# Kernel optimization log

Hardware: AMD Instinct MI355X
Metric: run time of the kernel (lower is better)

## Reference

```python
import jax, jax.numpy as jnp
import numpy as np

N_NODES = 50000
N_EDGES = 800000
N_FEAT = 128
N_HID = 256
N_PAIRS = 100000


def _gcn_norm(edge_index, n_nodes):
    # add self loops, compute D^-1/2 (A+I) D^-1/2 edge weights (PyG gcn_norm)
    loops = jnp.arange(n_nodes, dtype=edge_index.dtype)
    row = jnp.concatenate([edge_index[0], loops])
    col = jnp.concatenate([edge_index[1], loops])
    deg = jax.ops.segment_sum(jnp.ones_like(col, dtype=jnp.float32), col,
                              num_segments=n_nodes)
    dinv = jnp.where(deg > 0, jax.lax.rsqrt(deg), 0.0)
    norm = dinv[row] * dinv[col]  # [E + N]
    return row, col, norm


def _gcn_conv(x, W, b, row, col, norm, n_nodes):
    h = x @ W                       # [N, out]
    msg = h[row] * norm[:, None]    # gather + scale  [E+N, out]
    agg = jax.ops.segment_sum(msg, col, num_segments=n_nodes)  # scatter-add
    return agg + b


def setup_inputs() -> dict:
    key = jax.random.key(0)
    ks = jax.random.split(key, 9)
    edge_index = jax.random.randint(ks[0], (2, N_EDGES), 0, N_NODES, dtype=jnp.int64)
    features = jax.random.normal(ks[1], (N_NODES, N_FEAT), dtype=jnp.float32)
    mask = jax.random.randint(ks[2], (N_PAIRS, 2), 0, N_NODES, dtype=jnp.int64)
    s1 = 1.0 / np.sqrt(N_FEAT)
    s2 = 1.0 / np.sqrt(N_HID)
    W1 = jax.random.uniform(ks[3], (N_FEAT, N_HID), jnp.float32, -s1, s1)
    b1 = jnp.zeros((N_HID,), jnp.float32)
    W2 = jax.random.uniform(ks[4], (N_HID, N_FEAT), jnp.float32, -s2, s2)
    b2 = jnp.zeros((N_FEAT,), jnp.float32)
    Wl = jax.random.uniform(ks[5], (N_HID, 1), jnp.float32, -s2, s2)
    bl = jax.random.uniform(ks[6], (1,), jnp.float32, -s2, s2)
    return {"edge_index": edge_index, "features": features, "mask": mask,
            "W1": W1, "b1": b1, "W2": W2, "b2": b2, "Wl": Wl, "bl": bl}


def reference(edge_index, features, mask, W1, b1, W2, b2, Wl, bl):
    n = features.shape[0]
    row, col, norm = _gcn_norm(edge_index, n)
    h = _gcn_conv(features, W1, b1, row, col, norm, n)   # GCNConv a
    h = jax.nn.relu(h)                                   # dropout p=0 -> identity
    h = _gcn_conv(h, W2, b2, row, col, norm, n)          # GCNConv b
    mt = mask.T
    p1 = jax.lax.stop_gradient(h[mt[0]])                 # .detach()
    p2 = jax.lax.stop_gradient(h[mt[1]])
    hp = jnp.concatenate([p1, p2], axis=1)               # [n_pairs, 2*n_feat]
    return jax.nn.sigmoid(hp @ Wl + bl)
```

## Files before the change

### kernel.cpp

```cpp
#include <hip/hip_runtime.h>
#include <math.h>

#define NFEAT 128
#define NHID 256
#define NBLK 256

typedef __attribute__((ext_vector_type(8))) short short8;
typedef __attribute__((ext_vector_type(4))) float f32x4;
typedef __attribute__((ext_vector_type(2))) float f32x2;

__device__ inline unsigned short f2bf(float f) {
  unsigned u = __float_as_uint(f);
  u += 0x7fffu + ((u >> 16) & 1u);
  return (unsigned short)(u >> 16);
}
__device__ inline float bflo(unsigned u) { return __uint_as_float(u << 16); }
__device__ inline float bfhi(unsigned u) { return __uint_as_float(u & 0xffff0000u); }


__device__ inline void packOne(const float* __restrict__ W,
                               unsigned short* __restrict__ Wp, int idx, int KS,
                               int OUT) {
  int lane = idx & 63;
  int t = idx >> 6;
  int ks = t % KS;
  int nt = t / KS;
  int n = nt * 16 + (lane & 15);
  int k0 = ks * 32 + (lane >> 4) * 8;
  unsigned short v[8];
#pragma unroll
  for (int j = 0; j < 8; j++) v[j] = f2bf(W[(size_t)(k0 + j) * OUT + n]);
  *reinterpret_cast<short8*>(Wp + (size_t)idx * 8) =
      *reinterpret_cast<short8*>(v);
}

__global__ __launch_bounds__(1024) void k_hist_pack(
    const int* __restrict__ col, int* __restrict__ hist2d, int nE, int nb,
    const float* __restrict__ W1, const float* __restrict__ W2,
    unsigned short* __restrict__ W1p, unsigned short* __restrict__ W2p) {
  if (blockIdx.x >= NBLK) {
    int idx = (blockIdx.x - NBLK) * 1024 + threadIdx.x;
    if (idx < 4096) packOne(W1, W1p, idx, 4, 256);
    else packOne(W2, W2p, idx - 4096, 8, 128);
    return;
  }
  __shared__ int h[1024];
  for (int i = threadIdx.x; i < nb; i += 1024) h[i] = 0;
  __syncthreads();
  int chunk = (nE + NBLK - 1) / NBLK;
  int beg = blockIdx.x * chunk, end = min(beg + chunk, nE);
  for (int e = beg + threadIdx.x; e < end; e += 1024)
    atomicAdd(&h[col[e] >> 6], 1);
  __syncthreads();
  for (int i = threadIdx.x; i < nb; i += 1024)
    hist2d[i * NBLK + blockIdx.x] = h[i];
}

__global__ __launch_bounds__(256) void k_bsum(const int* __restrict__ a,
                                              int* __restrict__ psum, int S,
                                              const float* __restrict__ b2,
                                              const float* __restrict__ Wl,
                                              const float* __restrict__ bl,
                                              float* __restrict__ Cbuf) {
  int t = threadIdx.x;
  if (blockIdx.x == gridDim.x - 1) {
    float v = (t < 128) ? b2[t] * (Wl[t] + Wl[128 + t]) : 0.f;
#pragma unroll
    for (int o = 32; o; o >>= 1) v += __shfl_down(v, o);
    __shared__ float fw[4];
    if ((t & 63) == 0) fw[t >> 6] = v;
    __syncthreads();
    if (t == 0) Cbuf[0] = fw[0] + fw[1] + fw[2] + fw[3] + bl[0];
    return;
  }
  int i = blockIdx.x * 256 + t;
  int v = (i < S) ? a[i] : 0;
#pragma unroll
  for (int o = 32; o; o >>= 1) v += __shfl_down(v, o);
  __shared__ int ws[4];
  if ((t & 63) == 0) ws[t >> 6] = v;
  __syncthreads();
  if (t == 0) psum[blockIdx.x] = ws[0] + ws[1] + ws[2] + ws[3];
}

__global__ __launch_bounds__(256) void k_s3m(const int* __restrict__ a,
                                             const int* __restrict__ psum,
                                             int* __restrict__ out, int S) {
  __shared__ int sh[256];
  __shared__ int ws[4];
  int t = threadIdx.x;
  int b = blockIdx.x;
  int partial = 0;
  for (int i = t; i < b; i += 256) partial += psum[i];
#pragma unroll
  for (int o = 32; o; o >>= 1) partial += __shfl_down(partial, o);
  if ((t & 63) == 0) ws[t >> 6] = partial;
  int i = b * 256 + t;
  int d = (i < S) ? a[i] : 0;
  sh[t] = d;
  __syncthreads();
  int base = ws[0] + ws[1] + ws[2] + ws[3];
  for (int o = 1; o < 256; o <<= 1) {
    int u = (t >= o) ? sh[t - o] : 0;
    __syncthreads();
    sh[t] += u;
    __syncthreads();
  }
  if (i < S) out[i] = base + sh[t] - d;
}

__global__ __launch_bounds__(1024) void k_part2(const int* __restrict__ row,
                                                const int* __restrict__ col,
                                                const int* __restrict__ sbase,
                                                unsigned* __restrict__ tmp,
                                                int nE, int nb) {
  __shared__ int cur[1024];
  for (int i = threadIdx.x; i < nb; i += 1024)
    cur[i] = sbase[i * NBLK + blockIdx.x];
  __syncthreads();
  int chunk = (nE + NBLK - 1) / NBLK;
  int beg = blockIdx.x * chunk, end = min(beg + chunk, nE);
  for (int e = beg + threadIdx.x; e < end; e += 1024) {
    int c = col[e];
    int pos = atomicAdd(&cur[c >> 6], 1);
    tmp[pos] = ((unsigned)(c & 63) << 16) | (unsigned)row[e];
  }
}

__global__ __launch_bounds__(256) void k_bsort_cvt(
    const unsigned* __restrict__ tmp, const int* __restrict__ sbase,
    int* __restrict__ ebuf, int* __restrict__ offs, float* __restrict__ dinv,
    const float* __restrict__ feat, unsigned short* __restrict__ xs, int n,
    int nE, int nb) {
  __shared__ int bins[4][64], cur4[4][64];
  __shared__ float sdinv[64];
  int b = blockIdx.x;
  int beg = sbase[b * NBLK];
  int end = (b == nb - 1) ? nE : sbase[(b + 1) * NBLK];
  int t = threadIdx.x;
  int w4 = t >> 6;
  if (t == 0 && b == nb - 1) offs[n] = nE;
  bins[w4][t & 63] = 0;
  __syncthreads();
  for (int i = beg + t; i < end; i += 256)
    atomicAdd(&bins[w4][tmp[i] >> 16], 1);
  __syncthreads();
  if (t < 64) {
    int b0 = bins[0][t], b1 = bins[1][t], b2 = bins[2][t], b3 = bins[3][t];
    int v = b0 + b1 + b2 + b3;
    int s = v;
#pragma unroll
    for (int o = 1; o < 64; o <<= 1) {
      int u = __shfl_up(s, o);
      if (t >= o) s += u;
    }
    int off = beg + s - v;
    cur4[0][t] = off;
    cur4[1][t] = off + b0;
    cur4[2][t] = off + b0 + b1;
    cur4[3][t] = off + b0 + b1 + b2;
    float dv = rsqrtf((float)(v + 1));
    sdinv[t] = dv;
    int node = b * 64 + t;
    if (node < n) {
      offs[node] = off;
      dinv[node] = dv;
    }
  }
  __syncthreads();
  for (int i = beg + t; i < end; i += 256) {
    unsigned p = tmp[i];
    int pos = atomicAdd(&cur4[w4][p >> 16], 1);
    ebuf[pos] = (int)(p & 0xffffu);
  }
  for (int i = t; i < 64 * 32; i += 256) {
    int r = i >> 5;
    int node = b * 64 + r;
    if (node >= n) break;
    float d = sdinv[r];
    float4 v = reinterpret_cast<const float4*>(feat)[(size_t)node * 32 + (i & 31)];
    unsigned short o[4] = {f2bf(v.x * d), f2bf(v.y * d), f2bf(v.z * d),
                           f2bf(v.w * d)};
    reinterpret_cast<ushort4*>(xs)[(size_t)node * 32 + (i & 31)] =
        *reinterpret_cast<ushort4*>(o);
  }
}

#define ACC2(A, V)                        \
  A[0] += (f32x2){bflo(V.x), bfhi(V.x)};  \
  A[1] += (f32x2){bflo(V.y), bfhi(V.y)};  \
  A[2] += (f32x2){bflo(V.z), bfhi(V.z)};  \
  A[3] += (f32x2){bflo(V.w), bfhi(V.w)};

__global__ __launch_bounds__(256) void k_fused(
    const char* __restrict__ Gb, const int* __restrict__ offs,
    const int* __restrict__ ebuf, const float* __restrict__ dinv,
    const unsigned short* __restrict__ B1p, const unsigned short* __restrict__ B2p,
    const float* __restrict__ b1, const float* __restrict__ Wl,
    float* __restrict__ P, int n) {
  __shared__ __align__(16) unsigned short sh[32 * 264];
  __shared__ float pacc[32][2];
  int rt0 = blockIdx.x * 2;
  int wave = threadIdx.x >> 6;
  int lane = threadIdx.x & 63;
  int quad = lane >> 4;
  if (threadIdx.x < 64) pacc[threadIdx.x >> 1][threadIdx.x & 1] = 0.f;

  {
    int g = lane >> 4;
    int cidx = lane & 15;
    unsigned cb = (unsigned)cidx << 4;
    int rbase = rt0 * 16;
    for (int it = 0; it < 8; ++it) {
      int rin = wave * 8 + it;
      int node = rbase + rin;
      f32x2 acc[4] = {};
      float d = 0.f;
      if (node < n) {
        d = dinv[node];
        int beg = offs[node], end = offs[node + 1];
        int deg = end - beg;
        if (g == 0) {
          uint4 s = *reinterpret_cast<const uint4*>(
              Gb + (((unsigned)node << 8) | cb));
          ACC2(acc, s);
        }
        int kb = 0;
        while (kb < deg) {
          int m = min(deg - kb, 64);
          int myi = beg + kb + lane;
          int idx = (myi < end) ? ebuf[myi] : 0;
          int j = 0;
          for (; j + 16 <= m; j += 16) {
            int s0 = __shfl(idx, j + g);
            int s1 = __shfl(idx, j + 4 + g);
            int s2 = __shfl(idx, j + 8 + g);
            int s3 = __shfl(idx, j + 12 + g);
            uint4 v0 = *reinterpret_cast<const uint4*>(Gb + (((unsigned)s0 << 8) | cb));
            uint4 v1 = *reinterpret_cast<const uint4*>(Gb + (((unsigned)s1 << 8) | cb));
            uint4 v2 = *reinterpret_cast<const uint4*>(Gb + (((unsigned)s2 << 8) | cb));
            uint4 v3 = *reinterpret_cast<const uint4*>(Gb + (((unsigned)s3 << 8) | cb));
            ACC2(acc, v0);
            ACC2(acc, v1);
            ACC2(acc, v2);
            ACC2(acc, v3);
          }
          for (; j + 4 <= m; j += 4) {
            int s0 = __shfl(idx, j + g);
            uint4 v0 = *reinterpret_cast<const uint4*>(Gb + (((unsigned)s0 << 8) | cb));
            ACC2(acc, v0);
          }
          int r = m - j;
          if (r > 0) {
            int s0 = __shfl(idx, j + ((g < r) ? g : 0));
            if (g < r) {
              uint4 v0 = *reinterpret_cast<const uint4*>(Gb + (((unsigned)s0 << 8) | cb));
              ACC2(acc, v0);
            }
          }
          kb += 64;
        }
      }
#pragma unroll
      for (int j = 0; j < 4; j++) {
        acc[j].x += __shfl_down(acc[j].x, 32);
        acc[j].y += __shfl_down(acc[j].y, 32);
        acc[j].x += __shfl_down(acc[j].x, 16);
        acc[j].y += __shfl_down(acc[j].y, 16);
      }
      if (g == 0) {
        unsigned o[4];
#pragma unroll
        for (int k = 0; k < 4; k++)
          o[k] = (unsigned)f2bf(acc[k].x * d) |
                 ((unsigned)f2bf(acc[k].y * d) << 16);
        *reinterpret_cast<uint4*>(sh + rin * 128 + (cidx ^ (rin & 7)) * 8) =
            *reinterpret_cast<uint4*>(o);
      }
    }
  }
  __syncthreads();

  int r0a = lane & 15;
  int xsw = lane & 7;
  short8 fa0[4], fa1[4];
#pragma unroll
  for (int ks = 0; ks < 4; ks++) {
    int cS = ((quad + ks * 4) ^ xsw) * 8;
    fa0[ks] = *reinterpret_cast<const short8*>(sh + r0a * 128 + cS);
    fa1[ks] = *reinterpret_cast<const short8*>(sh + (16 + r0a) * 128 + cS);
  }
  __syncthreads();

  f32x4 acc[2][4] = {};
#pragma unroll
  for (int ks = 0; ks < 4; ks++) {
#pragma unroll
    for (int ct = 0; ct < 4; ct++) {
      int nt = wave * 4 + ct;
      short8 b = *reinterpret_cast<const short8*>(
          B1p + ((size_t)(nt * 4 + ks) * 64 + lane) * 8);
      acc[0][ct] = __builtin_amdgcn_mfma_f32_16x16x32_bf16(fa0[ks], b, acc[0][ct], 0, 0, 0);
      acc[1][ct] = __builtin_amdgcn_mfma_f32_16x16x32_bf16(fa1[ks], b, acc[1][ct], 0, 0, 0);
    }
  }
#pragma unroll
  for (int ct = 0; ct < 4; ct++) {
    int c = (wave * 4 + ct) * 16 + (lane & 15);
    float bv = b1[c];
#pragma unroll
    for (int rg = 0; rg < 2; rg++)
#pragma unroll
      for (int i = 0; i < 4; i++) {
        float v = fmaxf(acc[rg][ct][i] + bv, 0.f);
        sh[(rg * 16 + quad * 4 + i) * 264 + c] = f2bf(v);
      }
  }
  __syncthreads();

  f32x4 acc2[2][2] = {};
  const unsigned short* a2_0 = sh + (size_t)(lane & 15) * 264 + quad * 8;
  const unsigned short* a2_1 = sh + (size_t)(16 + (lane & 15)) * 264 + quad * 8;
#pragma unroll
  for (int ks = 0; ks < 8; ks++) {
    short8 a0 = *reinterpret_cast<const short8*>(a2_0 + ks * 32);
    short8 a1 = *reinterpret_cast<const short8*>(a2_1 + ks * 32);
#pragma unroll
    for (int ct = 0; ct < 2; ct++) {
      int nt = wave * 2 + ct;
      short8 b = *reinterpret_cast<const short8*>(
          B2p + ((size_t)(nt * 8 + ks) * 64 + lane) * 8);
      acc2[0][ct] = __builtin_amdgcn_mfma_f32_16x16x32_bf16(a0, b, acc2[0][ct], 0, 0, 0);
      acc2[1][ct] = __builtin_amdgcn_mfma_f32_16x16x32_bf16(a1, b, acc2[1][ct], 0, 0, 0);
    }
  }
  float p1[2][4] = {}, p2[2][4] = {};
#pragma unroll
  for (int rg = 0; rg < 2; rg++) {
    int r0 = (rt0 + rg) * 16 + quad * 4;
    float dv[4];
#pragma unroll
    for (int i = 0; i < 4; i++) dv[i] = dinv[r0 + i];
#pragma unroll
    for (int ct = 0; ct < 2; ct++) {
      int c = (wave * 2 + ct) * 16 + (lane & 15);
      float wl1 = Wl[c], wl2 = Wl[128 + c];
#pragma unroll
      for (int i = 0; i < 4; i++) {
        float v = acc2[rg][ct][i] * dv[i];
        p1[rg][i] = fmaf(v, wl1, p1[rg][i]);
        p2[rg][i] = fmaf(v, wl2, p2[rg][i]);
      }
    }
  }
#pragma unroll
  for (int rg = 0; rg < 2; rg++)
#pragma unroll
    for (int i = 0; i < 4; i++) {
#pragma unroll
      for (int o = 8; o; o >>= 1) {
        p1[rg][i] += __shfl_xor(p1[rg][i], o);
        p2[rg][i] += __shfl_xor(p2[rg][i], o);
      }
    }
  if ((lane & 15) == 0) {
#pragma unroll
    for (int rg = 0; rg < 2; rg++)
#pragma unroll
      for (int i = 0; i < 4; i++) {
        int row = rg * 16 + quad * 4 + i;
        atomicAdd(&pacc[row][0], p1[rg][i]);
        atomicAdd(&pacc[row][1], p2[rg][i]);
      }
  }
  __syncthreads();
  if (threadIdx.x < 64) {
    int row = threadIdx.x >> 1, comp = threadIdx.x & 1;
    P[(size_t)(rt0 * 16 + row) * 2 + comp] = pacc[row][comp];
  }
}

__global__ __launch_bounds__(256) void k_agg_s(const float2* __restrict__ p,
                                               const int* __restrict__ offs,
                                               const int* __restrict__ ebuf,
                                               const float* __restrict__ dinv,
                                               float2* __restrict__ q, int n) {
  int i = blockIdx.x * 64 + (threadIdx.x >> 2);
  if (i >= n) return;
  int sub = threadIdx.x & 3;
  int beg = offs[i], end = offs[i + 1];
  float sx = 0.f, sy = 0.f;
  for (int e = beg + sub; e < end; e += 4) {
    float2 v = p[ebuf[e]];
    sx += v.x;
    sy += v.y;
  }
  sx += __shfl_down(sx, 2);
  sy += __shfl_down(sy, 2);
  sx += __shfl_down(sx, 1);
  sy += __shfl_down(sy, 1);
  if (sub == 0) {
    float2 self = p[i];
    float d = dinv[i];
    q[i] = make_float2((sx + self.x) * d, (sy + self.y) * d);
  }
}

__global__ __launch_bounds__(256) void k_head2(const float2* __restrict__ q,
                                               const int* __restrict__ mask,
                                               const float* __restrict__ Cbuf,
                                               float* __restrict__ out, int P) {
  int p = blockIdx.x * 256 + threadIdx.x;
  if (p >= P) return;
  int m0 = mask[2 * p], m1 = mask[2 * p + 1];
  float s = q[m0].x + q[m1].y + Cbuf[0];
  out[p] = 1.0f / (1.0f + expf(-s));
}

extern "C" void kernel_launch(void* const* d_in, const int* in_sizes, int n_in,
                              void* d_out, int out_size, void* d_ws,
                              size_t ws_size, hipStream_t stream) {
  const int* edge = (const int*)d_in[0];
  const float* feat = (const float*)d_in[1];
  const int* mask = (const int*)d_in[2];
  const float* W1 = (const float*)d_in[3];
  const float* b1 = (const float*)d_in[4];
  const float* W2 = (const float*)d_in[5];
  const float* b2 = (const float*)d_in[6];
  const float* Wl = (const float*)d_in[7];
  const float* bl = (const float*)d_in[8];
  float* out = (float*)d_out;

  const int E = in_sizes[0] / 2;
  const int N = in_sizes[1] / NFEAT;
  const int P = in_sizes[2] / 2;
  const int* rowp = edge;
  const int* colp = edge + E;
  const int nrt = N / 16;
  const int nb = (N + 63) / 64;
  const int S = nb * NBLK;
  const int nS = (S + 255) / 256;

  auto aln = [](size_t x) { return (x + 255) & ~(size_t)255; };
  char* w = (char*)d_ws;
  int* hist2d = (int*)w;           w += aln((size_t)S * 4);
  int* sbase = (int*)w;            w += aln((size_t)S * 4);
  int* psum = (int*)w;             w += aln((size_t)1024 * 4);
  float* Cbuf = (float*)w;         w += aln(256);
  int* offs = (int*)w;             w += aln((size_t)(N + 1) * 4);
  int* ebuf = (int*)w;             w += aln((size_t)E * 4);
  unsigned* tmp = (unsigned*)w;    w += aln((size_t)E * 4);
  float* dinv = (float*)w;         w += aln((size_t)N * 4 + 1024);
  unsigned short* xs = (unsigned short*)w;  w += aln((size_t)N * NFEAT * 2);
  float* p = (float*)w;            w += aln((size_t)(N + 32) * 8);
  float2* q = (float2*)w;          w += aln((size_t)N * 8);
  unsigned short* W1p = (unsigned short*)w; w += aln((size_t)NFEAT * NHID * 2);
  unsigned short* W2p = (unsigned short*)w; w += aln((size_t)NHID * NFEAT * 2);

  k_hist_pack<<<NBLK + 8, 1024, 0, stream>>>(colp, hist2d, E, nb, W1, W2, W1p,
                                             W2p);
  k_bsum<<<nS + 1, 256, 0, stream>>>(hist2d, psum, S, b2, Wl, bl, Cbuf);
  k_s3m<<<nS, 256, 0, stream>>>(hist2d, psum, sbase, S);
  k_part2<<<NBLK, 1024, 0, stream>>>(rowp, colp, sbase, tmp, E, nb);
  k_bsort_cvt<<<nb, 256, 0, stream>>>(tmp, sbase, ebuf, offs, dinv, feat, xs,
                                      N, E, nb);
  k_fused<<<(nrt + 1) / 2, 256, 0, stream>>>((const char*)xs, offs, ebuf, dinv,
                                             W1p, W2p, b1, Wl, p, N);
  k_agg_s<<<(N + 63) / 64, 256, 0, stream>>>((const float2*)p, offs, ebuf,
                                             dinv, q, N);
  k_head2<<<(P + 255) / 256, 256, 0, stream>>>(q, mask, Cbuf, out, P);
}
```

Baseline: 179.0 us.

## Replace global CSR build with per-chunk local offsets and in-block edge bucketing

Drops the global two-level scan and the final CSR sort. Each partition block now scans its own histogram to produce chunk-local offsets, so tmp is only partitioned within each source chunk. The fused GEMM kernel and the aggregation kernel rebucket edges per 64-node bucket in shared memory, reading the 256 chunk segments directly. This removes three launches and one full edge pass plus the offs/ebuf writes. In exchange it adds per-block segment walking with atomics, and a slow fallback path when a bucket half exceeds ECAP edges.

```diff
diff --git a/kernel.cpp b/kernel.cpp
--- a/kernel.cpp
+++ b/kernel.cpp
@@ -4,6 +4,7 @@
 #define NFEAT 128
 #define NHID 256
 #define NBLK 256
+#define ECAP 3072
 
 typedef __attribute__((ext_vector_type(8))) short short8;
 typedef __attribute__((ext_vector_type(4))) float f32x4;
@@ -16,7 +17,6 @@
 }
 __device__ inline float bflo(unsigned u) { return __uint_as_float(u << 16); }
 __device__ inline float bfhi(unsigned u) { return __uint_as_float(u & 0xffff0000u); }
-
 
 __device__ inline void packOne(const float* __restrict__ W,
                                unsigned short* __restrict__ Wp, int idx, int KS,
@@ -34,155 +34,102 @@
       *reinterpret_cast<short8*>(v);
 }
 
-__global__ __launch_bounds__(1024) void k_hist_pack(
-    const int* __restrict__ col, int* __restrict__ hist2d, int nE, int nb,
+__global__ __launch_bounds__(1024) void k_hist2(
+    const int* __restrict__ col, int* __restrict__ sbase2, int nE, int nb,
     const float* __restrict__ W1, const float* __restrict__ W2,
-    unsigned short* __restrict__ W1p, unsigned short* __restrict__ W2p) {
+    unsigned short* __restrict__ W1p, unsigned short* __restrict__ W2p,
+    const float* __restrict__ b2, const float* __restrict__ Wl,
+    const float* __restrict__ bl, float* __restrict__ Cbuf) {
+  int t = threadIdx.x;
   if (blockIdx.x >= NBLK) {
-    int idx = (blockIdx.x - NBLK) * 1024 + threadIdx.x;
-    if (idx < 4096) packOne(W1, W1p, idx, 4, 256);
-    else packOne(W2, W2p, idx - 4096, 8, 128);
+    int sb = blockIdx.x - NBLK;
+    if (sb < 8) {
+      int idx = sb * 1024 + t;
+      if (idx < 4096) packOne(W1, W1p, idx, 4, 256);
+      else packOne(W2, W2p, idx - 4096, 8, 128);
+    } else {
+      float v = (t < 128) ? b2[t] * (Wl[t] + Wl[128 + t]) : 0.f;
+#pragma unroll
+      for (int o = 32; o; o >>= 1) v += __shfl_down(v, o);
+      __shared__ float fw[16];
+      if ((t & 63) == 0) fw[t >> 6] = v;
+      __syncthreads();
+      if (t == 0) {
+        float s = 0.f;
+        for (int i = 0; i < 16; i++) s += fw[i];
+        Cbuf[0] = s + bl[0];
+      }
+    }
     return;
   }
   __shared__ int h[1024];
-  for (int i = threadIdx.x; i < nb; i += 1024) h[i] = 0;
+  h[t] = 0;
   __syncthreads();
   int chunk = (nE + NBLK - 1) / NBLK;
   int beg = blockIdx.x * chunk, end = min(beg + chunk, nE);
-  for (int e = beg + threadIdx.x; e < end; e += 1024)
-    atomicAdd(&h[col[e] >> 6], 1);
-  __syncthreads();
-  for (int i = threadIdx.x; i < nb; i += 1024)
-    hist2d[i * NBLK + blockIdx.x] = h[i];
-}
-
-__global__ __launch_bounds__(256) void k_bsum(const int* __restrict__ a,
-                                              int* __restrict__ psum, int S,
-                                              const float* __restrict__ b2,
-                                              const float* __restrict__ Wl,
-                                              const float* __restrict__ bl,
-                                              float* __restrict__ Cbuf) {
-  int t = threadIdx.x;
-  if (blockIdx.x == gridDim.x - 1) {
-    float v = (t < 128) ? b2[t] * (Wl[t] + Wl[128 + t]) : 0.f;
-#pragma unroll
-    for (int o = 32; o; o >>= 1) v += __shfl_down(v, o);
-    __shared__ float fw[4];
-    if ((t & 63) == 0) fw[t >> 6] = v;
+  for (int e = beg + t; e < end; e += 1024) atomicAdd(&h[col[e] >> 6], 1);
+  __syncthreads();
+  int v = h[t];
+  for (int o = 1; o < 1024; o <<= 1) {
+    int u = (t >= o) ? h[t - o] : 0;
     __syncthreads();
-    if (t == 0) Cbuf[0] = fw[0] + fw[1] + fw[2] + fw[3] + bl[0];
-    return;
-  }
-  int i = blockIdx.x * 256 + t;
-  int v = (i < S) ? a[i] : 0;
-#pragma unroll
-  for (int o = 32; o; o >>= 1) v += __shfl_down(v, o);
-  __shared__ int ws[4];
-  if ((t & 63) == 0) ws[t >> 6] = v;
-  __syncthreads();
-  if (t == 0) psum[blockIdx.x] = ws[0] + ws[1] + ws[2] + ws[3];
-}
-
-__global__ __launch_bounds__(256) void k_s3m(const int* __restrict__ a,
-                                             const int* __restrict__ psum,
-                                             int* __restrict__ out, int S) {
-  __shared__ int sh[256];
-  __shared__ int ws[4];
-  int t = threadIdx.x;
-  int b = blockIdx.x;
-  int partial = 0;
-  for (int i = t; i < b; i += 256) partial += psum[i];
-#pragma unroll
-  for (int o = 32; o; o >>= 1) partial += __shfl_down(partial, o);
-  if ((t & 63) == 0) ws[t >> 6] = partial;
-  int i = b * 256 + t;
-  int d = (i < S) ? a[i] : 0;
-  sh[t] = d;
-  __syncthreads();
-  int base = ws[0] + ws[1] + ws[2] + ws[3];
-  for (int o = 1; o < 256; o <<= 1) {
-    int u = (t >= o) ? sh[t - o] : 0;
+    h[t] += u;
     __syncthreads();
-    sh[t] += u;
-    __syncthreads();
-  }
-  if (i < S) out[i] = base + sh[t] - d;
-}
-
-__global__ __launch_bounds__(1024) void k_part2(const int* __restrict__ row,
-                                                const int* __restrict__ col,
-                                                const int* __restrict__ sbase,
-                                                unsigned* __restrict__ tmp,
-                                                int nE, int nb) {
+  }
+  if (t < nb) sbase2[t * NBLK + blockIdx.x] = beg + h[t] - v;
+}
+
+__global__ __launch_bounds__(1024) void k_part2b(
+    const int* __restrict__ row, const int* __restrict__ col,
+    const int* __restrict__ sbase2, unsigned* __restrict__ tmp, int nE,
+    int nb) {
   __shared__ int cur[1024];
-  for (int i = threadIdx.x; i < nb; i += 1024)
-    cur[i] = sbase[i * NBLK + blockIdx.x];
+  int t = threadIdx.x, b = blockIdx.x;
+  for (int k = t; k < nb; k += 1024) cur[k] = sbase2[k * NBLK + b];
   __syncthreads();
   int chunk = (nE + NBLK - 1) / NBLK;
-  int beg = blockIdx.x * chunk, end = min(beg + chunk, nE);
-  for (int e = beg + threadIdx.x; e < end; e += 1024) {
+  int beg = b * chunk, end = min(beg + chunk, nE);
+  for (int e = beg + t; e < end; e += 1024) {
     int c = col[e];
     int pos = atomicAdd(&cur[c >> 6], 1);
     tmp[pos] = ((unsigned)(c & 63) << 16) | (unsigned)row[e];
   }
 }
 
-__global__ __launch_bounds__(256) void k_bsort_cvt(
-    const unsigned* __restrict__ tmp, const int* __restrict__ sbase,
-    int* __restrict__ ebuf, int* __restrict__ offs, float* __restrict__ dinv,
-    const float* __restrict__ feat, unsigned short* __restrict__ xs, int n,
-    int nE, int nb) {
-  __shared__ int bins[4][64], cur4[4][64];
+__global__ __launch_bounds__(256) void k_degcvt(
+    const unsigned* __restrict__ tmp, const int* __restrict__ sbase2,
+    float* __restrict__ dinv, const float* __restrict__ feat,
+    unsigned short* __restrict__ xs, int n, int nE, int nb) {
+  __shared__ int bins[4][64];
   __shared__ float sdinv[64];
-  int b = blockIdx.x;
-  int beg = sbase[b * NBLK];
-  int end = (b == nb - 1) ? nE : sbase[(b + 1) * NBLK];
-  int t = threadIdx.x;
-  int w4 = t >> 6;
-  if (t == 0 && b == nb - 1) offs[n] = nE;
-  bins[w4][t & 63] = 0;
-  __syncthreads();
-  for (int i = beg + t; i < end; i += 256)
-    atomicAdd(&bins[w4][tmp[i] >> 16], 1);
+  int t = threadIdx.x, k = blockIdx.x, w = t >> 6;
+  bins[w][t & 63] = 0;
+  __syncthreads();
+  int chunk = (nE + NBLK - 1) / NBLK;
+  int lo = sbase2[k * NBLK + t];
+  int hi = (k < nb - 1) ? sbase2[(k + 1) * NBLK + t] : min((t + 1) * chunk, nE);
+  for (int e = lo; e < hi; e++) atomicAdd(&bins[w][tmp[e] >> 16], 1);
   __syncthreads();
   if (t < 64) {
-    int b0 = bins[0][t], b1 = bins[1][t], b2 = bins[2][t], b3 = bins[3][t];
-    int v = b0 + b1 + b2 + b3;
-    int s = v;
-#pragma unroll
-    for (int o = 1; o < 64; o <<= 1) {
-      int u = __shfl_up(s, o);
-      if (t >= o) s += u;
-    }
-    int off = beg + s - v;
-    cur4[0][t] = off;
-    cur4[1][t] = off + b0;
-    cur4[2][t] = off + b0 + b1;
-    cur4[3][t] = off + b0 + b1 + b2;
-    float dv = rsqrtf((float)(v + 1));
+    int tot = bins[0][t] + bins[1][t] + bins[2][t] + bins[3][t];
+    float dv = rsqrtf((float)(tot + 1));
     sdinv[t] = dv;
-    int node = b * 64 + t;
-    if (node < n) {
-      offs[node] = off;
-      dinv[node] = dv;
-    }
-  }
-  __syncthreads();
-  for (int i = beg + t; i < end; i += 256) {
-    unsigned p = tmp[i];
-    int pos = atomicAdd(&cur4[w4][p >> 16], 1);
-    ebuf[pos] = (int)(p & 0xffffu);
-  }
+    int node = k * 64 + t;
+    if (node < n) dinv[node] = dv;
+  }
+  __syncthreads();
   for (int i = t; i < 64 * 32; i += 256) {
     int r = i >> 5;
-    int node = b * 64 + r;
-    if (node >= n) break;
-    float d = sdinv[r];
-    float4 v = reinterpret_cast<const float4*>(feat)[(size_t)node * 32 + (i & 31)];
-    unsigned short o[4] = {f2bf(v.x * d), f2bf(v.y * d), f2bf(v.z * d),
-                           f2bf(v.w * d)};
-    reinterpret_cast<ushort4*>(xs)[(size_t)node * 32 + (i & 31)] =
-        *reinterpret_cast<ushort4*>(o);
+    int node = k * 64 + r;
+    if (node < n) {
+      float d = sdinv[r];
+      float4 v =
+          reinterpret_cast<const float4*>(feat)[(size_t)node * 32 + (i & 31)];
+      unsigned short o[4] = {f2bf(v.x * d), f2bf(v.y * d), f2bf(v.z * d),
+                             f2bf(v.w * d)};
+      reinterpret_cast<ushort4*>(xs)[(size_t)node * 32 + (i & 31)] =
+          *reinterpret_cast<ushort4*>(o);
+    }
   }
 }
 
@@ -193,72 +140,121 @@
   A[3] += (f32x2){bflo(V.w), bfhi(V.w)};
 
 __global__ __launch_bounds__(256) void k_fused(
-    const char* __restrict__ Gb, const int* __restrict__ offs,
-    const int* __restrict__ ebuf, const float* __restrict__ dinv,
-    const unsigned short* __restrict__ B1p, const unsigned short* __restrict__ B2p,
-    const float* __restrict__ b1, const float* __restrict__ Wl,
-    float* __restrict__ P, int n) {
+    const char* __restrict__ Gb, const unsigned* __restrict__ tmp,
+    const int* __restrict__ sbase2, const unsigned short* __restrict__ B1p,
+    const unsigned short* __restrict__ B2p, const float* __restrict__ b1,
+    const float* __restrict__ Wl, float* __restrict__ P, int n, int nE,
+    int nb) {
   __shared__ __align__(16) unsigned short sh[32 * 264];
+  __shared__ int bins4[4][32], cur4[4][32], lbeg[33];
+  __shared__ float sdvL[32];
   __shared__ float pacc[32][2];
-  int rt0 = blockIdx.x * 2;
-  int wave = threadIdx.x >> 6;
-  int lane = threadIdx.x & 63;
-  int quad = lane >> 4;
-  if (threadIdx.x < 64) pacc[threadIdx.x >> 1][threadIdx.x & 1] = 0.f;
+  __shared__ int fbF;
+  int t = threadIdx.x;
+  int bucket = blockIdx.x >> 1, based = (blockIdx.x & 1) * 32;
+  int wave = t >> 6, lane = t & 63, quad = lane >> 4;
+  if (t < 64) pacc[t >> 1][t & 1] = 0.f;
+  if (t < 32) {
+    bins4[0][t] = 0; bins4[1][t] = 0; bins4[2][t] = 0; bins4[3][t] = 0;
+  }
+  if (t == 0) fbF = 0;
+  int chunk = (nE + NBLK - 1) / NBLK;
+  int lo = sbase2[bucket * NBLK + t];
+  int hi = (bucket < nb - 1) ? sbase2[(bucket + 1) * NBLK + t]
+                             : min((t + 1) * chunk, nE);
+  __syncthreads();
+  for (int e = lo; e < hi; e++) {
+    int dp = (int)(tmp[e] >> 16) - based;
+    if ((unsigned)dp < 32u) atomicAdd(&bins4[wave][dp], 1);
+  }
+  __syncthreads();
+  if (t < 32) {
+    int b0 = bins4[0][t], b1_ = bins4[1][t], b2_ = bins4[2][t],
+        b3_ = bins4[3][t];
+    int tot = b0 + b1_ + b2_ + b3_;
+    int s = tot;
+#pragma unroll
+    for (int o = 1; o < 32; o <<= 1) {
+      int u = __shfl_up(s, o);
+      if (t >= o) s += u;
+    }
+    int excl = s - tot;
+    lbeg[t] = excl;
+    if (t == 31) {
+      lbeg[32] = s;
+      if (s > ECAP) fbF = 1;
+    }
+    cur4[0][t] = excl;
+    cur4[1][t] = excl + b0;
+    cur4[2][t] = excl + b0 + b1_;
+    cur4[3][t] = excl + b0 + b1_ + b2_;
+    sdvL[t] = rsqrtf((float)(tot + 1));
+  }
+  __syncthreads();
+  int fb = fbF;
+  if (!fb) {
+    for (int e = lo; e < hi; e++) {
+      unsigned v = tmp[e];
+      int dp = (int)(v >> 16) - based;
+      if ((unsigned)dp < 32u) {
+        int pos = atomicAdd(&cur4[wave][dp], 1);
+        sh[pos] = (unsigned short)(v & 0xffffu);
+      }
+    }
+  } else {
+    int* segb = (int*)sh;
+    segb[t] = lo;
+    segb[256 + t] = hi;
+  }
+  __syncthreads();
 
   {
     int g = lane >> 4;
     int cidx = lane & 15;
     unsigned cb = (unsigned)cidx << 4;
-    int rbase = rt0 * 16;
     for (int it = 0; it < 8; ++it) {
       int rin = wave * 8 + it;
-      int node = rbase + rin;
+      int node = bucket * 64 + based + rin;
       f32x2 acc[4] = {};
-      float d = 0.f;
+      float dsc = 0.f;
       if (node < n) {
-        d = dinv[node];
-        int beg = offs[node], end = offs[node + 1];
-        int deg = end - beg;
+        dsc = sdvL[rin];
         if (g == 0) {
-          uint4 s = *reinterpret_cast<const uint4*>(
+          uint4 s0 = *reinterpret_cast<const uint4*>(
               Gb + (((unsigned)node << 8) | cb));
-          ACC2(acc, s);
+          ACC2(acc, s0);
         }
-        int kb = 0;
-        while (kb < deg) {
-          int m = min(deg - kb, 64);
-          int myi = beg + kb + lane;
-          int idx = (myi < end) ? ebuf[myi] : 0;
-          int j = 0;
-          for (; j + 16 <= m; j += 16) {
-            int s0 = __shfl(idx, j + g);
-            int s1 = __shfl(idx, j + 4 + g);
-            int s2 = __shfl(idx, j + 8 + g);
-            int s3 = __shfl(idx, j + 12 + g);
-            uint4 v0 = *reinterpret_cast<const uint4*>(Gb + (((unsigned)s0 << 8) | cb));
-            uint4 v1 = *reinterpret_cast<const uint4*>(Gb + (((unsigned)s1 << 8) | cb));
-            uint4 v2 = *reinterpret_cast<const uint4*>(Gb + (((unsigned)s2 << 8) | cb));
-            uint4 v3 = *reinterpret_cast<const uint4*>(Gb + (((unsigned)s3 << 8) | cb));
+        if (!fb) {
+          int e = lbeg[rin] + g, eh = lbeg[rin + 1];
+          for (; e + 4 < eh; e += 8) {
+            int s0 = sh[e], s1 = sh[e + 4];
+            uint4 v0 = *reinterpret_cast<const uint4*>(
+                Gb + (((unsigned)s0 << 8) | cb));
+            uint4 v1 = *reinterpret_cast<const uint4*>(
+                Gb + (((unsigned)s1 << 8) | cb));
             ACC2(acc, v0);
             ACC2(acc, v1);
-            ACC2(acc, v2);
-            ACC2(acc, v3);
           }
-          for (; j + 4 <= m; j += 4) {
-            int s0 = __shfl(idx, j + g);
-            uint4 v0 = *reinterpret_cast<const uint4*>(Gb + (((unsigned)s0 << 8) | cb));
+          if (e < eh) {
+            int s0 = sh[e];
+            uint4 v0 = *reinterpret_cast<const uint4*>(
+                Gb + (((unsigned)s0 << 8) | cb));
             ACC2(acc, v0);
           }
-          int r = m - j;
-          if (r > 0) {
-            int s0 = __shfl(idx, j + ((g < r) ? g : 0));
-            if (g < r) {
-              uint4 v0 = *reinterpret_cast<const uint4*>(Gb + (((unsigned)s0 << 8) | cb));
-              ACC2(acc, v0);
+        } else {
+          const int* segb = (const int*)sh;
+          int target = based + rin;
+          for (int s2 = 0; s2 < 256; s2++) {
+            int jl = segb[s2], jh = segb[256 + s2];
+            for (int j = jl + g; j < jh; j += 4) {
+              unsigned v = tmp[j];
+              if ((int)(v >> 16) == target) {
+                uint4 v0 = *reinterpret_cast<const uint4*>(
+                    Gb + (((v & 0xffffu) << 8) | cb));
+                ACC2(acc, v0);
+              }
             }
           }
-          kb += 64;
         }
       }
 #pragma unroll
@@ -271,10 +267,11 @@
       if (g == 0) {
         unsigned o[4];
 #pragma unroll
-        for (int k = 0; k < 4; k++)
-          o[k] = (unsigned)f2bf(acc[k].x * d) |
-                 ((unsigned)f2bf(acc[k].y * d) << 16);
-        *reinterpret_cast<uint4*>(sh + rin * 128 + (cidx ^ (rin & 7)) * 8) =
+        for (int k2 = 0; k2 < 4; k2++)
+          o[k2] = (unsigned)f2bf(acc[k2].x * dsc) |
+                  ((unsigned)f2bf(acc[k2].y * dsc) << 16);
+        *reinterpret_cast<uint4*>(sh + 4096 + rin * 128 +
+                                  (cidx ^ (rin & 7)) * 8) =
             *reinterpret_cast<uint4*>(o);
       }
     }
@@ -287,8 +284,9 @@
 #pragma unroll
   for (int ks = 0; ks < 4; ks++) {
     int cS = ((quad + ks * 4) ^ xsw) * 8;
-    fa0[ks] = *reinterpret_cast<const short8*>(sh + r0a * 128 + cS);
-    fa1[ks] = *reinterpret_cast<const short8*>(sh + (16 + r0a) * 128 + cS);
+    fa0[ks] = *reinterpret_cast<const short8*>(sh + 4096 + r0a * 128 + cS);
+    fa1[ks] =
+        *reinterpret_cast<const short8*>(sh + 4096 + (16 + r0a) * 128 + cS);
   }
   __syncthreads();
 
@@ -337,17 +335,13 @@
   float p1[2][4] = {}, p2[2][4] = {};
 #pragma unroll
   for (int rg = 0; rg < 2; rg++) {
-    int r0 = (rt0 + rg) * 16 + quad * 4;
-    float dv[4];
-#pragma unroll
-    for (int i = 0; i < 4; i++) dv[i] = dinv[r0 + i];
 #pragma unroll
     for (int ct = 0; ct < 2; ct++) {
       int c = (wave * 2 + ct) * 16 + (lane & 15);
       float wl1 = Wl[c], wl2 = Wl[128 + c];
 #pragma unroll
       for (int i = 0; i < 4; i++) {
-        float v = acc2[rg][ct][i] * dv[i];
+        float v = acc2[rg][ct][i] * sdvL[rg * 16 + quad * 4 + i];
         p1[rg][i] = fmaf(v, wl1, p1[rg][i]);
         p2[rg][i] = fmaf(v, wl2, p2[rg][i]);
       }
@@ -374,35 +368,41 @@
       }
   }
   __syncthreads();
-  if (threadIdx.x < 64) {
-    int row = threadIdx.x >> 1, comp = threadIdx.x & 1;
-    P[(size_t)(rt0 * 16 + row) * 2 + comp] = pacc[row][comp];
-  }
-}
-
-__global__ __launch_bounds__(256) void k_agg_s(const float2* __restrict__ p,
-                                               const int* __restrict__ offs,
-                                               const int* __restrict__ ebuf,
-                                               const float* __restrict__ dinv,
-                                               float2* __restrict__ q, int n) {
-  int i = blockIdx.x * 64 + (threadIdx.x >> 2);
-  if (i >= n) return;
-  int sub = threadIdx.x & 3;
-  int beg = offs[i], end = offs[i + 1];
-  float sx = 0.f, sy = 0.f;
-  for (int e = beg + sub; e < end; e += 4) {
-    float2 v = p[ebuf[e]];
-    sx += v.x;
-    sy += v.y;
-  }
-  sx += __shfl_down(sx, 2);
-  sy += __shfl_down(sy, 2);
-  sx += __shfl_down(sx, 1);
-  sy += __shfl_down(sy, 1);
-  if (sub == 0) {
-    float2 self = p[i];
-    float d = dinv[i];
-    q[i] = make_float2((sx + self.x) * d, (sy + self.y) * d);
+  if (t < 64) {
+    int row = t >> 1, comp = t & 1;
+    P[(size_t)(blockIdx.x * 32 + row) * 2 + comp] = pacc[row][comp];
+  }
+}
+
+__global__ __launch_bounds__(256) void k_aggs(
+    const float2* __restrict__ p, const unsigned* __restrict__ tmp,
+    const int* __restrict__ sbase2, const float* __restrict__ dinv,
+    float2* __restrict__ q, int n, int nE, int nb) {
+  __shared__ float pacc[64][2];
+  int t = threadIdx.x, k = blockIdx.x;
+  if (t < 64) {
+    pacc[t][0] = 0.f;
+    pacc[t][1] = 0.f;
+  }
+  __syncthreads();
+  int chunk = (nE + NBLK - 1) / NBLK;
+  int lo = sbase2[k * NBLK + t];
+  int hi = (k < nb - 1) ? sbase2[(k + 1) * NBLK + t] : min((t + 1) * chunk, nE);
+  for (int e = lo; e < hi; e++) {
+    unsigned v = tmp[e];
+    float2 pv = p[v & 0xffffu];
+    atomicAdd(&pacc[v >> 16][0], pv.x);
+    atomicAdd(&pacc[v >> 16][1], pv.y);
+  }
+  __syncthreads();
+  if (t < 64) {
+    int node = k * 64 + t;
+    if (node < n) {
+      float2 self = p[node];
+      float d = dinv[node];
+      q[node] = make_float2((pacc[t][0] + self.x) * d,
+                            (pacc[t][1] + self.y) * d);
+    }
   }
 }
 
@@ -436,37 +436,28 @@
   const int P = in_sizes[2] / 2;
   const int* rowp = edge;
   const int* colp = edge + E;
-  const int nrt = N / 16;
   const int nb = (N + 63) / 64;
   const int S = nb * NBLK;
-  const int nS = (S + 255) / 256;
 
   auto aln = [](size_t x) { return (x + 255) & ~(size_t)255; };
   char* w = (char*)d_ws;
-  int* hist2d = (int*)w;           w += aln((size_t)S * 4);
-  int* sbase = (int*)w;            w += aln((size_t)S * 4);
-  int* psum = (int*)w;             w += aln((size_t)1024 * 4);
+  int* sbase2 = (int*)w;           w += aln((size_t)S * 4);
   float* Cbuf = (float*)w;         w += aln(256);
-  int* offs = (int*)w;             w += aln((size_t)(N + 1) * 4);
-  int* ebuf = (int*)w;             w += aln((size_t)E * 4);
   unsigned* tmp = (unsigned*)w;    w += aln((size_t)E * 4);
   float* dinv = (float*)w;         w += aln((size_t)N * 4 + 1024);
   unsigned short* xs = (unsigned short*)w;  w += aln((size_t)N * NFEAT * 2);
-  float* p = (float*)w;            w += aln((size_t)(N + 32) * 8);
+  float* p = (float*)w;            w += aln((size_t)nb * 64 * 8);
   float2* q = (float2*)w;          w += aln((size_t)N * 8);
   unsigned short* W1p = (unsigned short*)w; w += aln((size_t)NFEAT * NHID * 2);
   unsigned short* W2p = (unsigned short*)w; w += aln((size_t)NHID * NFEAT * 2);
 
-  k_hist_pack<<<NBLK + 8, 1024, 0, stream>>>(colp, hist2d, E, nb, W1, W2, W1p,
-                                             W2p);
-  k_bsum<<<nS + 1, 256, 0, stream>>>(hist2d, psum, S, b2, Wl, bl, Cbuf);
-  k_s3m<<<nS, 256, 0, stream>>>(hist2d, psum, sbase, S);
-  k_part2<<<NBLK, 1024, 0, stream>>>(rowp, colp, sbase, tmp, E, nb);
-  k_bsort_cvt<<<nb, 256, 0, stream>>>(tmp, sbase, ebuf, offs, dinv, feat, xs,
-                                      N, E, nb);
-  k_fused<<<(nrt + 1) / 2, 256, 0, stream>>>((const char*)xs, offs, ebuf, dinv,
-                                             W1p, W2p, b1, Wl, p, N);
-  k_agg_s<<<(N + 63) / 64, 256, 0, stream>>>((const float2*)p, offs, ebuf,
-                                             dinv, q, N);
+  k_hist2<<<NBLK + 9, 1024, 0, stream>>>(colp, sbase2, E, nb, W1, W2, W1p,
+                                         W2p, b2, Wl, bl, Cbuf);
+  k_part2b<<<NBLK, 1024, 0, stream>>>(rowp, colp, sbase2, tmp, E, nb);
+  k_degcvt<<<nb, 256, 0, stream>>>(tmp, sbase2, dinv, feat, xs, N, E, nb);
+  k_fused<<<nb * 2, 256, 0, stream>>>((const char*)xs, tmp, sbase2, W1p, W2p,
+                                      b1, Wl, p, N, E, nb);
+  k_aggs<<<nb, 256, 0, stream>>>((const float2*)p, tmp, sbase2, dinv, q, N, E,
+                                 nb);
   k_head2<<<(P + 255) / 256, 256, 0, stream>>>(q, mask, Cbuf, out, P);
 }
```

After: 197.1 us. 1.1x slower.
